# Performance work log

Hardware: AMD Instinct MI355X
Metric: run time of the kernel (lower is better)

## Reference

```python
import jax, jax.numpy as jnp
import numpy as np

DMODEL = 1024

def setup_inputs() -> dict:
    key = jax.random.key(0)
    ks = jax.random.split(key, 7)
    scale = 1.0 / np.sqrt(DMODEL)
    x = jax.random.normal(ks[0], (4, 2048, DMODEL), dtype=jnp.float32)
    Wq = jax.random.normal(ks[1], (DMODEL, DMODEL), dtype=jnp.float32) * scale
    bq = jnp.zeros((DMODEL,), dtype=jnp.float32)
    Wk = jax.random.normal(ks[2], (DMODEL, DMODEL), dtype=jnp.float32) * scale
    bk = jnp.zeros((DMODEL,), dtype=jnp.float32)
    Wv = jax.random.normal(ks[3], (DMODEL, DMODEL), dtype=jnp.float32) * scale
    bv = jnp.zeros((DMODEL,), dtype=jnp.float32)
    return {"x": x, "Wq": Wq, "bq": bq, "Wk": Wk, "bk": bk, "Wv": Wv, "bv": bv}

def reference(x, Wq, bq, Wk, bk, Wv, bv):
    # QKV projections: [b, s, d]
    q = jnp.einsum('bsd,de->bse', x, Wq) + bq
    k = jnp.einsum('bsd,de->bse', x, Wk) + bk
    v = jnp.einsum('bsd,de->bse', x, Wv) + bv
    # scaled dot-product attention, full [b, s, s] score matrix (as in source)
    scores = jnp.einsum('bqd,bkd->bqk', q, k) / jnp.sqrt(jnp.asarray(q.shape[-1], q.dtype))
    weights = jax.nn.softmax(scores, axis=-1)
    return jnp.einsum('bqk,bkd->bqd', weights, v)
```

## Files before the change

kernel.cpp:

```cpp
#include <hip/hip_runtime.h>

typedef unsigned short u16;
typedef __attribute__((ext_vector_type(8))) short short8;
typedef __attribute__((ext_vector_type(4))) short short4v;
typedef __attribute__((ext_vector_type(4))) float f32x4;


__device__ __forceinline__ u16 f2bf(float f) {
  union { float f; unsigned u; } c; c.f = f;
  unsigned u = c.u;
  unsigned r = u + 0x7fffu + ((u >> 16) & 1u);
  return (u16)(r >> 16);
}

__device__ __forceinline__ float bf2f(u16 b) {
  union { unsigned u; float f; } c; c.u = ((unsigned)b) << 16;
  return c.f;
}

__device__ __forceinline__ void load_lds16(const void* g, void* l) {
  __builtin_amdgcn_global_load_lds(
      (__attribute__((address_space(1))) void*)(__UINTPTR_TYPE__)(g),
      (__attribute__((address_space(3))) void*)(l),
      16, 0, 0);
}

template <int N> __device__ __forceinline__ void vm_wait() {
  if constexpr (N == 0) asm volatile("s_waitcnt vmcnt(0)" ::: "memory");
  else if constexpr (N == 3) asm volatile("s_waitcnt vmcnt(3)" ::: "memory");
  else if constexpr (N == 4) asm volatile("s_waitcnt vmcnt(4)" ::: "memory");
}

template <int BM, int MODE>
__global__ __launch_bounds__(512)
void gemm256(const u16* __restrict__ A, const u16* __restrict__ Bt,
             void* __restrict__ C0, void* __restrict__ C1,
             const float* __restrict__ b0, const float* __restrict__ b1,
             const float* __restrict__ b2,
             int K, int lda, int ldb, int ldc, float scale,
             long zsA, long zsB, long zsC)
{
  constexpr int MREP = BM / 32;
  constexpr int H    = MREP / 2;
  constexpr int LA   = BM / 128;
  constexpr int BOFF = BM * 64;
  constexpr int LDSE = BM * 64 + 16384;
  __shared__ __align__(16) u16 lds[2][LDSE];

  A  += (long)blockIdx.z * zsA;
  Bt += (long)blockIdx.z * zsB;

  int bxi, byi;
  if (MODE == 0 || MODE == 3) {
    const int gw   = gridDim.x;
    const int nwg  = gw * gridDim.y;
    const int orig = blockIdx.x + gw * blockIdx.y;
    const int s    = (orig & 7) * (nwg >> 3) + (orig >> 3);
    bxi = s % gw; byi = s / gw;
  } else {
    bxi = blockIdx.x; byi = blockIdx.y;
  }

  const int t    = threadIdx.x;
  const int lane = t & 63;
  const int wave = t >> 6;
  const int wr   = wave >> 2;
  const int wc   = wave & 3;
  const long brow = (long)byi * BM;
  const long bcol = (long)bxi * 256;

  f32x4 acc[MREP][4];
#pragma unroll
  for (int m = 0; m < MREP; ++m)
#pragma unroll
    for (int n = 0; n < 4; ++n)
#pragma unroll
      for (int j = 0; j < 4; ++j) acc[m][n][j] = 0.f;

  const int frA  = wr * (BM / 2) + (lane & 15);
  const int kAsw = (((lane >> 4) ^ ((frA >> 1) & 3)) * 8);
  const int frB  = wc * 64 + (lane & 15);
  const int kBsw = (((lane >> 4) ^ ((frB >> 1) & 3)) * 8);

  const int sr  = t >> 2;
  const int ssl = ((t & 3) ^ ((sr >> 1) & 3)) * 8;
  const u16* gA = A  + (size_t)(brow + sr) * lda + ssl;
  const u16* gB = Bt + (size_t)(bcol + sr) * ldb + ssl;
  const int NT = K >> 6;

#define STAGE_A(nb, kt1, ks) do {                                   \
    u16* d = &lds[(nb)][(ks) * (BM * 32) + t * 8];                  \
    const u16* g = gA + (size_t)(kt1) * 64 + (ks) * 32;             \
    load_lds16(g, d);                                               \
    if (LA == 2) load_lds16(g + (size_t)128 * lda, d + 4096);       \
  } while (0)

#define STAGE_B(nb, kt1, ks) do {                                   \
    u16* d = &lds[(nb)][BOFF + (ks) * 8192 + t * 8];                \
    const u16* g = gB + (size_t)(kt1) * 64 + (ks) * 32;             \
    load_lds16(g, d);                                               \
    load_lds16(g + (size_t)128 * ldb, d + 4096);                    \
  } while (0)

#define PHASE(ks, mh, STG, VM) {                                                 \
    _Pragma("unroll")                                                            \
    for (int i = 0; i < H; ++i)                                                  \
      af[i] = *(const short8*)&bufA[(ks) * (BM * 32) +                           \
                 (size_t)(frA + ((mh) * H + i) * 16) * 32 + kAsw];               \
    if ((mh) == 0) {                                                             \
      _Pragma("unroll")                                                          \
      for (int n = 0; n < 4; ++n)                                                \
        bf[n] = *(const short8*)&bufB[(ks) * 8192 +                              \
                   (size_t)(frB + n * 16) * 32 + kBsw];                          \
    }                                                                            \
    STG;                                                                         \
    asm volatile("s_waitcnt lgkmcnt(0)" ::: "memory");                           \
    __builtin_amdgcn_sched_barrier(0);                                           \
    __builtin_amdgcn_s_setprio(1);                                               \
    _Pragma("unroll")                                                            \
    for (int i = 0; i < H; ++i)                                                  \
      _Pragma("unroll")                                                          \
      for (int n = 0; n < 4; ++n)                                                \
        acc[(mh) * H + i][n] = __builtin_amdgcn_mfma_f32_16x16x32_bf16(          \
            af[i], bf[n], acc[(mh) * H + i][n], 0, 0, 0);                        \
    __builtin_amdgcn_s_setprio(0);                                               \
    VM;                                                                          \
    asm volatile("s_barrier" ::: "memory");                                      \
  }

  STAGE_A(0, 0, 0); STAGE_B(0, 0, 0); STAGE_A(0, 0, 1); STAGE_B(0, 0, 1);
  vm_wait<0>();
  asm volatile("s_barrier" ::: "memory");

  short8 af[H], bf[4];
  for (int kt = 0; kt < NT - 1; ++kt) {
    const u16* bufA = &lds[kt & 1][0];
    const u16* bufB = bufA + BOFF;
    const int nb = (kt + 1) & 1;
    PHASE(0, 0, STAGE_A(nb, kt + 1, 0), (void)0)
    PHASE(0, 1, STAGE_B(nb, kt + 1, 0), vm_wait<LA + 2>())
    PHASE(1, 0, STAGE_A(nb, kt + 1, 1), (void)0)
    PHASE(1, 1, STAGE_B(nb, kt + 1, 1), vm_wait<LA + 2>())
  }
  {
    const u16* bufA = &lds[(NT - 1) & 1][0];
    const u16* bufB = bufA + BOFF;
    PHASE(0, 0, (void)0, (void)0)
    PHASE(0, 1, (void)0, vm_wait<0>())
    PHASE(1, 0, (void)0, (void)0)
    PHASE(1, 1, (void)0, (void)0)
  }
#undef PHASE
#undef STAGE_A
#undef STAGE_B

  const int dcol = lane & 15;
  const int dr4  = (lane >> 4) * 4;
  if (MODE == 0) {
    const int which = (int)(bcol >> 10);
    const float sc = which ? 1.0f : scale;
    const float* bb = which ? b1 : b0;
    u16* dst = (u16*)C0 + (long)which * (8192L * 1024);
#pragma unroll
    for (int m = 0; m < MREP; ++m) {
#pragma unroll
      for (int n = 0; n < 4; ++n) {
        const long cp   = (bcol - ((long)which << 10)) + wc * 64 + n * 16 + dcol;
        const long row0 = brow + wr * (BM / 2) + m * 16 + dr4;
        const float bias = bb[cp];
#pragma unroll
        for (int j = 0; j < 4; ++j)
          dst[(row0 + j) * 1024 + cp] = f2bf((acc[m][n][j] + bias) * sc);
      }
    }
  } else if (MODE == 3) {
    constexpr int SMSK = BM / 4 - 1;
    u16* sm = (u16*)lds;
#pragma unroll
    for (int m = 0; m < MREP; ++m) {
#pragma unroll
      for (int n = 0; n < 4; ++n) {
        const int cpl = wc * 64 + n * 16 + dcol;
        const int r0l = wr * (BM / 2) + m * 16 + dr4;
        const float bias = b2[bcol + cpl];
        short4v w;
#pragma unroll
        for (int j = 0; j < 4; ++j) w[j] = (short)f2bf(acc[m][n][j] + bias);
        *(short4v*)&sm[cpl * BM + (((r0l >> 2) ^ (cpl & SMSK)) << 2)] = w;
      }
    }
    __syncthreads();
    u16* dst = (u16*)C1;
#pragma unroll
    for (int it = 0; it < BM / 16; ++it) {
      const int idx = it * 512 + t;
      const int i  = idx / (BM / 8);
      const int ch = idx & (BM / 8 - 1);
      const short4v lo = *(const short4v*)&sm[i * BM + ((((ch * 2)    ) ^ (i & SMSK)) << 2)];
      const short4v hi = *(const short4v*)&sm[i * BM + ((((ch * 2) + 1) ^ (i & SMSK)) << 2)];
      short8 o;
      o[0] = lo[0]; o[1] = lo[1]; o[2] = lo[2]; o[3] = lo[3];
      o[4] = hi[0]; o[5] = hi[1]; o[6] = hi[2]; o[7] = hi[3];
      *(short8*)&dst[(bcol + i) * 8192 + brow + ch * 8] = o;
    }
  } else {
#pragma unroll
    for (int m = 0; m < MREP; ++m) {
#pragma unroll
      for (int n = 0; n < 4; ++n) {
        const long col  = bcol + wc * 64 + n * 16 + dcol;
        const long row0 = brow + wr * (BM / 2) + m * 16 + dr4;
        if (MODE == 1) {
#pragma unroll
          for (int j = 0; j < 4; ++j)
            ((u16*)C0)[(long)blockIdx.z * zsC + (row0 + j) * ldc + col] =
                f2bf(acc[m][n][j] * scale);
        } else {
#pragma unroll
          for (int j = 0; j < 4; ++j)
            ((float*)C0)[(long)blockIdx.z * zsC + (row0 + j) * ldc + col] =
                acc[m][n][j];
        }
      }
    }
  }
}

__global__ __launch_bounds__(256)
void cvt_bf16(const float* __restrict__ in, u16* __restrict__ out, int n4)
{
  int i = blockIdx.x * 256 + threadIdx.x;
  const int stride = gridDim.x * 256;
  for (; i < n4; i += stride) {
    const float4 f = ((const float4*)in)[i];
    ushort4 u;
    u.x = f2bf(f.x); u.y = f2bf(f.y); u.z = f2bf(f.z); u.w = f2bf(f.w);
    ((ushort4*)out)[i] = u;
  }
}

__global__ __launch_bounds__(256)
void wtrans(const float* __restrict__ W, u16* __restrict__ Wt)
{
  __shared__ u16 tile[32][33];
  const int tx = threadIdx.x;
  const int ty = threadIdx.y;
  const int bx = blockIdx.x * 32;
  const int by = blockIdx.y * 32;
#pragma unroll
  for (int i = 0; i < 4; ++i)
    tile[ty + i * 8][tx] = f2bf(W[(size_t)(by + ty + i * 8) * 1024 + bx + tx]);
  __syncthreads();
#pragma unroll
  for (int i = 0; i < 4; ++i)
    Wt[(size_t)(bx + ty + i * 8) * 1024 + by + tx] = tile[tx][ty + i * 8];
}

__global__ __launch_bounds__(256)
void softmax_rows_bf16(u16* __restrict__ S)
{
  u16* s = S + (size_t)blockIdx.x * 2048;
  const int t = threadIdx.x;

  const short8 r = ((const short8*)s)[t];
  float v[8];
#pragma unroll
  for (int i = 0; i < 8; ++i) v[i] = bf2f((u16)r[i]);

  float m = -1e30f;
#pragma unroll
  for (int i = 0; i < 8; ++i) m = fmaxf(m, v[i]);
#pragma unroll
  for (int o = 32; o; o >>= 1) m = fmaxf(m, __shfl_xor(m, o));
  __shared__ float redm[4], reds[4];
  if ((t & 63) == 0) redm[t >> 6] = m;
  __syncthreads();
  m = fmaxf(fmaxf(redm[0], redm[1]), fmaxf(redm[2], redm[3]));

  float sum = 0.f;
#pragma unroll
  for (int i = 0; i < 8; ++i) { v[i] = __expf(v[i] - m); sum += v[i]; }
#pragma unroll
  for (int o = 32; o; o >>= 1) sum += __shfl_xor(sum, o);
  if ((t & 63) == 0) reds[t >> 6] = sum;
  __syncthreads();
  const float inv = 1.f / (reds[0] + reds[1] + reds[2] + reds[3]);

  short8 w;
#pragma unroll
  for (int i = 0; i < 8; ++i) w[i] = (short)f2bf(v[i] * inv);
  ((short8*)s)[t] = w;
}

extern "C" void kernel_launch(void* const* d_in, const int* in_sizes, int n_in,
                              void* d_out, int out_size, void* d_ws, size_t ws_size,
                              hipStream_t stream)
{
  const float* x  = (const float*)d_in[0];
  const float* Wq = (const float*)d_in[1];
  const float* bq = (const float*)d_in[2];
  const float* Wk = (const float*)d_in[3];
  const float* bk = (const float*)d_in[4];
  const float* Wv = (const float*)d_in[5];
  const float* bv = (const float*)d_in[6];
  float* out = (float*)d_out;
  char* ws = (char*)d_ws;

  const size_t MB = (size_t)1 << 20;
  const float qscale = 0.03125f;
  const long  SO = 2048L * 1024;

  u16* Qb   = (u16*)(ws);
  u16* Kb   = (u16*)(ws + 16 * MB);
  u16* Vt   = (u16*)(ws + 32 * MB);
  u16* Sc   = (u16*)(ws + 48 * MB);
  u16* xb   = (u16*)(ws + 48 * MB);
  u16* Wcat = (u16*)(ws + 80 * MB);

  cvt_bf16<<<2048, 256, 0, stream>>>(x, xb, (4 * 2048 * 1024) / 4);
  dim3 tb(32, 8), tg(32, 32);
  wtrans<<<tg, tb, 0, stream>>>(Wq, Wcat);
  wtrans<<<tg, tb, 0, stream>>>(Wk, Wcat + 1024 * 1024);
  wtrans<<<tg, tb, 0, stream>>>(Wv, Wcat + 2 * 1024 * 1024);

  gemm256<256, 0><<<dim3(8, 32), 512, 0, stream>>>(
      xb, Wcat, Qb, nullptr, bq, bk, nullptr,
      1024, 1024, 1024, 1024, qscale, 0, 0, 0);

  gemm256<128, 3><<<dim3(4, 64), 512, 0, stream>>>(
      xb, Wcat + 2 * 1024 * 1024, nullptr, Vt, nullptr, nullptr, bv,
      1024, 1024, 1024, 1024, 1.0f, 0, 0, 0);

  gemm256<256, 1><<<dim3(8, 8, 4), 512, 0, stream>>>(
      Qb, Kb, Sc, nullptr, nullptr, nullptr, nullptr,
      1024, 1024, 1024, 2048, 1.0f, SO, SO, 2048L * 2048);

  softmax_rows_bf16<<<4 * 2048, 256, 0, stream>>>(Sc);

  gemm256<128, 2><<<dim3(4, 16, 4), 512, 0, stream>>>(
      Sc, Vt, out, nullptr, nullptr, nullptr, nullptr,
      2048, 2048, 8192, 1024, 1.0f, 2048L * 2048, 2048, SO);
}
```

Measured before the change: 174.0 us.

## Add dedicated 128x256 triple-buffered GEMM for attention score computation

Adds a new kernel, gemm_s32, for the Q·K^T score GEMM. It uses 128x256 block tiles with a K-step of 32 and a three-stage LDS ring buffer, replacing the 256x256 gemm256 launch with a grid of twice as many blocks. The aim is to raise occupancy and parallelism (launch bounds of 4) and overlap global-to-LDS loads with MFMA compute. It also inserts an extra s_barrier in the shared PHASE macro after staging, which adds synchronisation to the other GEMMs and may slow them.

```diff
diff --git a/kernel.cpp b/kernel.cpp
--- a/kernel.cpp
+++ b/kernel.cpp
@@ -114,6 +114,7 @@
                    (size_t)(frB + n * 16) * 32 + kBsw];                          \
     }                                                                            \
     STG;                                                                         \
+    asm volatile("s_barrier" ::: "memory");                                      \
     asm volatile("s_waitcnt lgkmcnt(0)" ::: "memory");                           \
     __builtin_amdgcn_sched_barrier(0);                                           \
     __builtin_amdgcn_s_setprio(1);                                               \
@@ -226,6 +227,97 @@
   }
 }
 
+__global__ __launch_bounds__(512, 4)
+void gemm_s32(const u16* __restrict__ A, const u16* __restrict__ Bt,
+              u16* __restrict__ C, int K, int lda, int ldb, int ldc,
+              long zsA, long zsB, long zsC)
+{
+  __shared__ __align__(16) u16 lds3[3][12288];
+
+  A  += (long)blockIdx.z * zsA;
+  Bt += (long)blockIdx.z * zsB;
+
+  const int t    = threadIdx.x;
+  const int lane = t & 63;
+  const int wave = t >> 6;
+  const int wr   = wave >> 2;
+  const int wc   = wave & 3;
+  const long brow = (long)blockIdx.y * 128;
+  const long bcol = (long)blockIdx.x * 256;
+
+  f32x4 acc[4][4];
+#pragma unroll
+  for (int m = 0; m < 4; ++m)
+#pragma unroll
+    for (int n = 0; n < 4; ++n)
+#pragma unroll
+      for (int j = 0; j < 4; ++j) acc[m][n][j] = 0.f;
+
+  const int frA  = wr * 64 + (lane & 15);
+  const int kAsw = (((lane >> 4) ^ ((frA >> 1) & 3)) * 8);
+  const int frB  = wc * 64 + (lane & 15);
+  const int kBsw = (((lane >> 4) ^ ((frB >> 1) & 3)) * 8);
+
+  const int sr  = t >> 2;
+  const int ssl = ((t & 3) ^ ((sr >> 1) & 3)) * 8;
+  const u16* gA = A  + (size_t)(brow + sr) * lda + ssl;
+  const u16* gB = Bt + (size_t)(bcol + sr) * ldb + ssl;
+  const int NT = K >> 5;
+
+#define SSTAGE(w, buf) do {                                         \
+    const size_t ko = (size_t)(w) * 32;                             \
+    load_lds16(gA + ko, &lds3[(buf)][t * 8]);                       \
+    load_lds16(gB + ko, &lds3[(buf)][4096 + t * 8]);                \
+    load_lds16(gB + ko + (size_t)128 * ldb, &lds3[(buf)][8192 + t * 8]); \
+  } while (0)
+
+  SSTAGE(0, 0);
+  SSTAGE(1, 1);
+  vm_wait<3>();
+  asm volatile("s_barrier" ::: "memory");
+
+  for (int kt = 0; kt < NT; ++kt) {
+    const u16* buf = &lds3[kt % 3][0];
+    short8 af[4], bfr[4];
+#pragma unroll
+    for (int m = 0; m < 4; ++m)
+      af[m] = *(const short8*)&buf[(size_t)(frA + m * 16) * 32 + kAsw];
+#pragma unroll
+    for (int n = 0; n < 4; ++n)
+      bfr[n] = *(const short8*)&buf[4096 + (size_t)(frB + n * 16) * 32 + kBsw];
+    if (kt + 2 < NT) SSTAGE(kt + 2, (kt + 2) % 3);
+
+    asm volatile("s_barrier" ::: "memory");
+    asm volatile("s_waitcnt lgkmcnt(0)" ::: "memory");
+    __builtin_amdgcn_sched_barrier(0);
+    __builtin_amdgcn_s_setprio(1);
+#pragma unroll
+    for (int m = 0; m < 4; ++m)
+#pragma unroll
+      for (int n = 0; n < 4; ++n)
+        acc[m][n] = __builtin_amdgcn_mfma_f32_16x16x32_bf16(af[m], bfr[n], acc[m][n], 0, 0, 0);
+    __builtin_amdgcn_s_setprio(0);
+    if (kt == NT - 2) vm_wait<0>();
+    else if (kt < NT - 2) vm_wait<3>();
+    asm volatile("s_barrier" ::: "memory");
+  }
+#undef SSTAGE
+
+  const int dcol = lane & 15;
+  const int dr4  = (lane >> 4) * 4;
+#pragma unroll
+  for (int m = 0; m < 4; ++m) {
+#pragma unroll
+    for (int n = 0; n < 4; ++n) {
+      const long col  = bcol + wc * 64 + n * 16 + dcol;
+      const long row0 = brow + wr * 64 + m * 16 + dr4;
+#pragma unroll
+      for (int j = 0; j < 4; ++j)
+        C[(long)blockIdx.z * zsC + (row0 + j) * ldc + col] = f2bf(acc[m][n][j]);
+    }
+  }
+}
+
 __global__ __launch_bounds__(256)
 void cvt_bf16(const float* __restrict__ in, u16* __restrict__ out, int n4)
 {
@@ -331,9 +423,8 @@
       xb, Wcat + 2 * 1024 * 1024, nullptr, Vt, nullptr, nullptr, bv,
       1024, 1024, 1024, 1024, 1.0f, 0, 0, 0);
 
-  gemm256<256, 1><<<dim3(8, 8, 4), 512, 0, stream>>>(
-      Qb, Kb, Sc, nullptr, nullptr, nullptr, nullptr,
-      1024, 1024, 1024, 2048, 1.0f, SO, SO, 2048L * 2048);
+  gemm_s32<<<dim3(8, 16, 4), 512, 0, stream>>>(
+      Qb, Kb, Sc, 1024, 1024, 1024, 2048, SO, SO, 2048L * 2048);
 
   softmax_rows_bf16<<<4 * 2048, 256, 0, stream>>>(Sc);
 
```

Result: slower. 182.7 us (+5.0%).
